# Performance work log

Measured on AMD Instinct MI355X. Metric: run time of the kernel, lower is better.

The kernel has to match this reference:

```python
import jax, jax.numpy as jnp
import numpy as np

H = 2048          # hidden_size
HEAD = 64         # head_size
NH = H // HEAD    # n_heads = 32
B, T = 4, 4096
LORA_MIX = 32     # per-branch rank of time_maa low-rank mixer (5 branches)
LORA_DECAY = 64   # rank of decay low-rank mixer


def setup_inputs() -> dict:
    key = jax.random.key(0)
    ks = jax.random.split(key, 24)
    s = 0.02  # small init scale keeps tanh/silu in sane range
    inp = {
        "hidden": jax.random.normal(ks[0], (B, T, H), jnp.float32),
        "attn_x": jax.random.normal(ks[1], (B, H), jnp.float32),
        "attn_kv": jax.random.normal(ks[2], (B, NH, HEAD, HEAD), jnp.float32),
        "ffn_x": jax.random.normal(ks[3], (B, H), jnp.float32),
        "time_maa_x": jax.random.normal(ks[4], (1, 1, H), jnp.float32) * s,
        "time_maa_w": jax.random.normal(ks[5], (1, 1, H), jnp.float32) * s,
        "time_maa_k": jax.random.normal(ks[6], (1, 1, H), jnp.float32) * s,
        "time_maa_v": jax.random.normal(ks[7], (1, 1, H), jnp.float32) * s,
        "time_maa_r": jax.random.normal(ks[8], (1, 1, H), jnp.float32) * s,
        "time_maa_g": jax.random.normal(ks[9], (1, 1, H), jnp.float32) * s,
        "time_maa_w1": jax.random.normal(ks[10], (H, LORA_MIX * 5), jnp.float32) * s,
        "time_maa_w2": jax.random.normal(ks[11], (5, LORA_MIX, H), jnp.float32) * s,
        "time_decay": jax.random.normal(ks[12], (1, 1, H), jnp.float32) * s,
        "time_decay_w1": jax.random.normal(ks[13], (H, LORA_DECAY), jnp.float32) * s,
        "time_decay_w2": jax.random.normal(ks[14], (LORA_DECAY, H), jnp.float32) * s,
        "time_faaaa": jax.random.normal(ks[15], (NH, HEAD), jnp.float32) * s,
        "receptance_w": jax.random.normal(ks[16], (H, H), jnp.float32) * s,
        "key_w": jax.random.normal(ks[17], (H, H), jnp.float32) * s,
        "value_w": jax.random.normal(ks[18], (H, H), jnp.float32) * s,
        "gate_w": jax.random.normal(ks[19], (H, H), jnp.float32) * s,
        "output_w": jax.random.normal(ks[20], (H, H), jnp.float32) * s,
    }
    return inp


def reference(hidden, attn_x, attn_kv, ffn_x,
              time_maa_x, time_maa_w, time_maa_k, time_maa_v, time_maa_r, time_maa_g,
              time_maa_w1, time_maa_w2,
              time_decay, time_decay_w1, time_decay_w2, time_faaaa,
              receptance_w, key_w, value_w, gate_w, output_w):
    b, t, h = hidden.shape
    # token shift: prepend previous chunk's last token state
    shifted = jnp.concatenate([attn_x[:, None, :], hidden[:, :-1, :]], axis=1)  # [B,T,H]
    x = hidden
    xx = shifted - x
    # low-rank data-dependent mixing coefficients (5 branches)
    xxx = x + xx * time_maa_x                                        # [B,T,H]
    xxx = jnp.tanh(xxx.reshape(-1, h) @ time_maa_w1)                 # [B*T, 5*32]
    xxx = xxx.reshape(-1, 5, LORA_MIX).transpose(1, 0, 2)            # [5, B*T, 32]
    xxx = jnp.einsum('fnr,frh->fnh', xxx, time_maa_w2)               # [5, B*T, H]
    xxx = xxx.reshape(5, b, t, h)
    mw, mk, mv, mr, mg = xxx[0], xxx[1], xxx[2], xxx[3], xxx[4]
    # note: source uses additive mix (x + xx + coeff), faithful to code as written
    td_in = x + xx + (time_maa_w + mw)
    k_in = x + xx + (time_maa_k + mk)
    v_in = x + xx + (time_maa_v + mv)
    r_in = x + xx + (time_maa_r + mr)
    g_in = x + xx + (time_maa_g + mg)
    receptance = jnp.einsum('bth,hd->btd', r_in, receptance_w)
    key = jnp.einsum('bth,hd->btd', k_in, key_w)
    value = jnp.einsum('bth,hd->btd', v_in, value_w)
    gate = jax.nn.silu(jnp.einsum('bth,hd->btd', g_in, gate_w))
    td = jnp.tanh(jnp.einsum('bth,hr->btr', td_in, time_decay_w1))
    td = jnp.einsum('btr,rh->bth', td, time_decay_w2)
    td = time_decay + td                                              # [B,T,H] per-channel decay
    attn_x_new = hidden[:, -1]                                        # [B,H]
    return (receptance, key, value, gate, td, attn_x_new)
```

## Files before the change

### kernel.cpp

```cpp
#include <hip/hip_runtime.h>

#define H 2048
#define TT 4096
#define BB 4
#define NROWS (BB * TT)
#define NTH ((size_t)NROWS * H)
#define KCAT (H + 32)
#define KC8  (H + 64)
#define NTH64 ((size_t)NROWS * 64)

typedef __attribute__((ext_vector_type(8))) short bh8;
typedef __attribute__((ext_vector_type(4))) float f32x4;

__device__ inline unsigned short f2bf(float f) {
    union { float f; unsigned u; } v; v.f = f;
    unsigned r = v.u + 0x7fff + ((v.u >> 16) & 1);
    return (unsigned short)(r >> 16);
}
__device__ inline float bf2f(unsigned short u) {
    union { unsigned u; float f; } v; v.u = ((unsigned)u) << 16; return v.f;
}
__device__ inline void gload_lds16(const void* g, void* l) {
    __builtin_amdgcn_global_load_lds(
        (const __attribute__((address_space(1))) void*)g,
        (__attribute__((address_space(3))) void*)l, 16, 0, 0);
}

__global__ __launch_bounds__(256) void prep_kernel(
    const float* __restrict__ hidden, const float* __restrict__ attn_x,
    const float* __restrict__ tmx,
    unsigned short* __restrict__ shifted, unsigned short* __restrict__ xin) {
    size_t i = ((size_t)blockIdx.x * 256 + threadIdx.x) * 4;
    int n = (int)(i >> 11);
    int h = (int)(i & 2047);
    int t = n & (TT - 1);
    float4 x = *(const float4*)(hidden + i);
    float4 s;
    if (t == 0) {
        int b = n >> 12;
        s = *(const float4*)(attn_x + ((size_t)b << 11) + h);
    } else {
        s = *(const float4*)(hidden + (i - H));
    }
    float4 m = *(const float4*)(tmx + h);
    ushort4 sh, xi;
    sh.x = f2bf(s.x); sh.y = f2bf(s.y); sh.z = f2bf(s.z); sh.w = f2bf(s.w);
    xi.x = f2bf(x.x + (s.x - x.x) * m.x);
    xi.y = f2bf(x.y + (s.y - x.y) * m.y);
    xi.z = f2bf(x.z + (s.z - x.z) * m.z);
    xi.w = f2bf(x.w + (s.w - x.w) * m.w);
    *(ushort4*)(shifted + i) = sh;
    *(ushort4*)(xin + i) = xi;
}

__global__ __launch_bounds__(256) void transpose_kernel(
    const float* __restrict__ in, unsigned short* __restrict__ outp,
    int R, int C, int ldo) {
    __shared__ float tile[32][33];
    int tx = threadIdx.x & 31, ty = threadIdx.x >> 5;
    int r0 = blockIdx.y * 32, c0 = blockIdx.x * 32;
    for (int i = ty; i < 32; i += 8) {
        int r = r0 + i, c = c0 + tx;
        tile[i][tx] = (r < R && c < C) ? in[(size_t)r * C + c] : 0.f;
    }
    __syncthreads();
    for (int i = ty; i < 32; i += 8) {
        int c = c0 + i, r = r0 + tx;
        if (c < C && r < R) outp[(size_t)c * ldo + r] = f2bf(tile[tx][i]);
    }
}

__global__ __launch_bounds__(256) void transpose4_kernel(
    const float* __restrict__ w0, const float* __restrict__ w1,
    const float* __restrict__ w2, const float* __restrict__ w3,
    unsigned short* __restrict__ d0, unsigned short* __restrict__ d1,
    unsigned short* __restrict__ d2, unsigned short* __restrict__ d3) {
    __shared__ float tile[32][33];
    int bz = blockIdx.z;
    const float* in = bz == 0 ? w0 : bz == 1 ? w1 : bz == 2 ? w2 : w3;
    unsigned short* outp = bz == 0 ? d0 : bz == 1 ? d1 : bz == 2 ? d2 : d3;
    int tx = threadIdx.x & 31, ty = threadIdx.x >> 5;
    int r0 = blockIdx.y * 32, c0 = blockIdx.x * 32;
    for (int i = ty; i < 32; i += 8)
        tile[i][tx] = in[(size_t)(r0 + i) * H + c0 + tx];
    __syncthreads();
    for (int i = ty; i < 32; i += 8)
        outp[(size_t)(c0 + i) * KC8 + r0 + tx] = f2bf(tile[tx][i]);
}

__global__ __launch_bounds__(256) void w2wp_kernel(
    const float* __restrict__ W2,
    const float* __restrict__ w0, const float* __restrict__ w1,
    const float* __restrict__ w2, const float* __restrict__ w3,
    const float* __restrict__ W1d,
    float* __restrict__ part) {
    const int br = blockIdx.z, ks = blockIdx.y, dblk = blockIdx.x;
    const int tid = threadIdx.x;
    const float* W; int D;
    if (br < 4) { W = br == 0 ? w0 : br == 1 ? w1 : br == 2 ? w2 : w3; D = H; }
    else        { W = W1d; D = 64; }
    const int f = br < 4 ? ((0x4213 >> (br * 4)) & 15) : 0;
    const float* W2f = W2 + (size_t)f * 32 * H;
    __shared__ float w2s[256][32];
    const int k0 = ks * 256;
    for (int idx = tid; idx < 8192; idx += 256) {
        int r = idx & 31, kk = idx >> 5;
        w2s[kk][r] = W2f[(size_t)r * H + k0 + kk];
    }
    __syncthreads();
    int d = dblk * 256 + tid;
    if (d >= D) return;
    float a[32];
#pragma unroll
    for (int r = 0; r < 32; ++r) a[r] = 0.f;
    for (int kk = 0; kk < 256; ++kk) {
        float w = W[(size_t)(k0 + kk) * D + d];
        const float4* w4 = (const float4*)w2s[kk];
#pragma unroll
        for (int rq = 0; rq < 8; ++rq) {
            float4 v = w4[rq];
            a[rq * 4 + 0] += v.x * w;
            a[rq * 4 + 1] += v.y * w;
            a[rq * 4 + 2] += v.z * w;
            a[rq * 4 + 3] += v.w * w;
        }
    }
    float* pp = part + (((size_t)br * 8 + ks) * 32) * 2048 + d;
#pragma unroll
    for (int r = 0; r < 32; ++r) pp[(size_t)r * 2048] = a[r];
}

__global__ __launch_bounds__(256) void w2wr_kernel(
    const float* __restrict__ part,
    unsigned short* __restrict__ dR, unsigned short* __restrict__ dK,
    unsigned short* __restrict__ dV, unsigned short* __restrict__ dG,
    unsigned short* __restrict__ d1) {
    int gid = blockIdx.x * 256 + threadIdx.x;
    if (gid < 262144) {
        int br = gid >> 16, rem = gid & 65535;
        int r = rem >> 11, d = rem & 2047;
        float s = 0.f;
#pragma unroll
        for (int ks = 0; ks < 8; ++ks)
            s += part[(((size_t)br * 8 + ks) * 32 + r) * 2048 + d];
        unsigned short* dst = br == 0 ? dR : br == 1 ? dK : br == 2 ? dV : dG;
        dst[(size_t)d * KC8 + H + r] = f2bf(s);
        dst[(size_t)d * KC8 + H + 32 + r] = 0;
    } else {
        int q = gid - 262144;
        int r = q >> 6, d = q & 63;
        float s = 0.f;
#pragma unroll
        for (int ks = 0; ks < 8; ++ks)
            s += part[(((size_t)4 * 8 + ks) * 32 + r) * 2048 + d];
        d1[(size_t)d * KCAT + H + r] = f2bf(s);
    }
}

__global__ __launch_bounds__(256) void bias_all_kernel(
    const unsigned short* __restrict__ bR, const unsigned short* __restrict__ bK,
    const unsigned short* __restrict__ bV, const unsigned short* __restrict__ bG,
    const unsigned short* __restrict__ b1,
    const float* __restrict__ mR, const float* __restrict__ mK,
    const float* __restrict__ mV, const float* __restrict__ mG,
    const float* __restrict__ mW,
    float* __restrict__ bias4, float* __restrict__ bias0) {
    int wave = threadIdx.x >> 6, lane = threadIdx.x & 63;
    int p = blockIdx.x * 4 + wave;
    const unsigned short* src; const float* maa; float* dst;
    if (p < 8192) {
        int br = p >> 11, row = p & 2047;
        src = (br == 0 ? bR : br == 1 ? bK : br == 2 ? bV : bG) + (size_t)row * KC8;
        maa = (br == 0 ? mR : br == 1 ? mK : br == 2 ? mV : mG);
        dst = bias4 + br * H + row;
    } else {
        int q = p - 8192;
        if (q >= 64) return;
        src = b1 + (size_t)q * KCAT; maa = mW; dst = bias0 + q;
    }
    float a = 0.f;
#pragma unroll 4
    for (int i = 0; i < 32; ++i) { int h = i * 64 + lane; a += bf2f(src[h]) * maa[h]; }
    for (int s = 32; s; s >>= 1) a += __shfl_xor(a, s);
    if (lane == 0) *dst = a;
}

template <int WM, int WN, int FM, int FN, int HAS_BIAS, int ACT, int OF32, int ZPAD>
__global__ __launch_bounds__(256) void gemm_kernel(
    const unsigned short* __restrict__ A, int lda,
    const unsigned short* __restrict__ A2, int lda2, int KS,
    const unsigned short* __restrict__ Bt, int ldb, int K,
    void* __restrict__ outp, int ldo, int NT,
    const float* __restrict__ bias) {
    static_assert(WM * WN == 4, "4 waves");
    constexpr int BM = WM * FM * 16;
    constexpr int BN = WN * FN * 16;
    __shared__ unsigned short As[BM * 32];
    __shared__ unsigned short Bs[BN * 32];

    const int nb = gridDim.x;
    const int bid = blockIdx.x;
    const int swz = (bid & 7) * (nb >> 3) + (bid >> 3);
    const int mt = swz / NT, nt = swz % NT;
    const int m0 = mt * BM, n0 = nt * BN;

    const int tid = threadIdx.x;
    const int wave = tid >> 6, lane = tid & 63;
    const int l16 = lane & 15, kh = lane >> 4;
    const int wr = wave / WN, wc = wave % WN;

    f32x4 acc[FM][FN] = {};

    constexpr int ACH = BM * 4;
    constexpr int BCH = BN * 4;

    for (int k0 = 0; k0 < K; k0 += 32) {
#pragma unroll
        for (int i = 0; i < (ACH + 255) / 256; ++i) {
            int c = i * 256 + tid;
            if (ACH % 256 == 0 || c < ACH) {
                int row = c >> 2, ck = c & 3;
                int kk = k0 + ck * 8;
                const unsigned short* gp = (kk < KS)
                    ? A  + (size_t)(m0 + row) * lda  + kk
                    : A2 + (size_t)(m0 + row) * lda2 + (kk - KS);
                gload_lds16(gp, As + (size_t)(i * 256 + wave * 64) * 8);
            }
        }
#pragma unroll
        for (int i = 0; i < (BCH + 255) / 256; ++i) {
            int c = i * 256 + tid;
            if (BCH % 256 == 0 || c < BCH) {
                int row = c >> 2, ck = c & 3;
                gload_lds16(Bt + (size_t)(n0 + row) * ldb + k0 + ck * 8,
                            Bs + (size_t)(i * 256 + wave * 64) * 8);
            }
        }
        __syncthreads();
        bh8 av[FM], bv[FN];
#pragma unroll
        for (int mi = 0; mi < FM; ++mi)
            av[mi] = *(const bh8*)((const char*)As + (((wr * FM + mi) * 16 + l16) * 64 + kh * 16));
#pragma unroll
        for (int ni = 0; ni < FN; ++ni)
            bv[ni] = *(const bh8*)((const char*)Bs + (((wc * FN + ni) * 16 + l16) * 64 + kh * 16));
#pragma unroll
        for (int mi = 0; mi < FM; ++mi)
#pragma unroll
            for (int ni = 0; ni < FN; ++ni)
                acc[mi][ni] = __builtin_amdgcn_mfma_f32_16x16x32_bf16(
                    av[mi], bv[ni], acc[mi][ni], 0, 0, 0);
        __syncthreads();
    }

#pragma unroll
    for (int mi = 0; mi < FM; ++mi) {
#pragma unroll
        for (int ni = 0; ni < FN; ++ni) {
            int col = n0 + (wc * FN + ni) * 16 + l16;
            float bcol = HAS_BIAS ? bias[col] : 0.f;
#pragma unroll
            for (int j = 0; j < 4; ++j) {
                int row = m0 + (wr * FM + mi) * 16 + kh * 4 + j;
                float v = acc[mi][ni][j] + bcol;
                if (ACT == 1) v = v * (1.f / (1.f + __expf(-v)));
                else if (ACT == 2) v = tanhf(v);
                if (ZPAD) {
                    int br = col >> 5, cc = col & 31;
                    unsigned short* zp = (unsigned short*)outp
                        + (size_t)br * NTH64 + (size_t)row * 64 + cc;
                    zp[0] = f2bf(v);
                    zp[32] = 0;
                } else if (OF32) {
                    ((float*)outp)[(size_t)row * ldo + col] = v;
                } else {
                    ((unsigned short*)outp)[(size_t)row * ldo + col] = f2bf(v);
                }
            }
        }
    }
}

__global__ __launch_bounds__(512, 2) void bigproj8_kernel(
    const unsigned short* __restrict__ A,
    const unsigned short* __restrict__ zpad,
    const unsigned short* __restrict__ bt0, const unsigned short* __restrict__ bt1,
    const unsigned short* __restrict__ bt2, const unsigned short* __restrict__ bt3,
    const float* __restrict__ bias4, float* __restrict__ out) {
    constexpr int BUFB = 65536;
    constexpr int NTK = KC8 / 64;
    __shared__ alignas(16) char lds[2 * BUFB];

    const int bid = blockIdx.x;
    const int swz = (bid & 7) * 256 + (bid >> 3);
    const int branch = swz >> 9;
    const int tile = swz & 511;
    const int m0 = (tile >> 3) * 256, n0 = (tile & 7) * 256;

    const unsigned short* Bt = branch == 0 ? bt0 : branch == 1 ? bt1
                             : branch == 2 ? bt2 : bt3;
    const int f = (0x4213 >> (branch * 4)) & 15;
    const unsigned short* Az = zpad + (size_t)f * NTH64;

    const int tid = threadIdx.x;
    const int wave = tid >> 6, lane = tid & 63;
    const int l16 = lane & 15, kh = lane >> 4;
    const int wm = wave >> 2, wn = wave & 3;
    const int kh16 = kh * 16;
    const int swr = (l16 & 8) << 2;

    const int rS = tid >> 2;
    const int kbx = ((tid & 3) * 16) ^ ((rS & 8) << 2);
    const char* bA0 = (const char*)A  + (size_t)(m0 + rS) * 4096 + kbx;
    const char* bA1 = bA0 + (size_t)128 * 4096;
    const char* bz0 = (const char*)Az + (size_t)(m0 + rS) * 128 + kbx;
    const char* bz1 = bz0 + (size_t)128 * 128;
    const char* bB0 = (const char*)Bt + (size_t)(n0 + rS) * (KC8 * 2) + kbx;
    const char* bB1 = bB0 + (size_t)128 * (KC8 * 2);
    const int dA0 = wave * 1024, dA1 = 8192 + wave * 1024;

    auto stageA = [&](int kt, char* nb) {
        const char *p0, *p1;
        if (kt < 32) { size_t o = (size_t)kt * 128; p0 = bA0 + o; p1 = bA1 + o; }
        else         { p0 = bz0; p1 = bz1; }
#pragma unroll
        for (int s = 0; s < 2; ++s) {
            gload_lds16(p0 + s * 64, nb + s * 16384 + dA0);
            gload_lds16(p1 + s * 64, nb + s * 16384 + dA1);
        }
    };
    auto stageB = [&](int kt, char* nb) {
        size_t o = (size_t)kt * 128;
#pragma unroll
        for (int s = 0; s < 2; ++s) {
            gload_lds16(bB0 + o + s * 64, nb + 32768 + s * 16384 + dA0);
            gload_lds16(bB1 + o + s * 64, nb + 32768 + s * 16384 + dA1);
        }
    };
    auto rdA = [&](const char* bb, int s, int g) {
        return *(const bh8*)(bb + s * 16384 + g * 1024 + l16 * 64 + (kh16 ^ swr));
    };
    auto rdB = [&](const char* bb, int s, int g) {
        return *(const bh8*)(bb + 32768 + s * 16384 + g * 1024 + l16 * 64 + (kh16 ^ swr));
    };

    f32x4 acc[8][4] = {};
    bh8 avX[4], avY[4], bv0[4], bv1[4];

    stageA(0, lds);        stageB(0, lds);
    stageA(1, lds + BUFB); stageB(1, lds + BUFB);
    asm volatile("s_waitcnt vmcnt(8)" ::: "memory");
    __builtin_amdgcn_s_barrier();
    __builtin_amdgcn_sched_barrier(0);
#pragma unroll
    for (int i = 0; i < 4; ++i) {
        avX[i] = rdA(lds, 0, wm * 8 + i);
        bv0[i] = rdB(lds, 0, wn * 4 + i);
    }

    for (int t = 0; t < NTK; ++t) {
        const char* cb = lds + (t & 1) * BUFB;
        char* sb = lds + (t & 1) * BUFB;
        const char* nxb = lds + ((t + 1) & 1) * BUFB;
        const bool hasNext = (t + 1) < NTK;
        const bool doSt = (t + 2) < NTK;

#pragma unroll
        for (int i = 0; i < 4; ++i) avY[i] = rdA(cb, 0, wm * 8 + 4 + i);
        __builtin_amdgcn_s_setprio(1);
#pragma unroll
        for (int mi = 0; mi < 4; ++mi)
#pragma unroll
            for (int ni = 0; ni < 4; ++ni)
                acc[mi][ni] = __builtin_amdgcn_mfma_f32_16x16x32_bf16(
                    avX[mi], bv0[ni], acc[mi][ni], 0, 0, 0);
        __builtin_amdgcn_s_setprio(0);

#pragma unroll
        for (int i = 0; i < 4; ++i) {
            avX[i] = rdA(cb, 1, wm * 8 + i);
            bv1[i] = rdB(cb, 1, wn * 4 + i);
        }
        __builtin_amdgcn_s_setprio(1);
#pragma unroll
        for (int mi = 0; mi < 4; ++mi)
#pragma unroll
            for (int ni = 0; ni < 4; ++ni)
                acc[4 + mi][ni] = __builtin_amdgcn_mfma_f32_16x16x32_bf16(
                    avY[mi], bv0[ni], acc[4 + mi][ni], 0, 0, 0);
        __builtin_amdgcn_s_setprio(0);

#pragma unroll
        for (int i = 0; i < 4; ++i) avY[i] = rdA(cb, 1, wm * 8 + 4 + i);
        __builtin_amdgcn_s_setprio(1);
#pragma unroll
        for (int mi = 0; mi < 4; ++mi)
#pragma unroll
            for (int ni = 0; ni < 4; ++ni)
                acc[mi][ni] = __builtin_amdgcn_mfma_f32_16x16x32_bf16(
                    avX[mi], bv1[ni], acc[mi][ni], 0, 0, 0);
        __builtin_amdgcn_s_setprio(0);

        if (hasNext) {
            asm volatile("s_waitcnt vmcnt(0) lgkmcnt(0)" ::: "memory");
            __builtin_amdgcn_s_barrier();
            __builtin_amdgcn_sched_barrier(0);
            if (doSt) { stageA(t + 2, sb); stageB(t + 2, sb); }
#pragma unroll
            for (int i = 0; i < 4; ++i) {
                avX[i] = rdA(nxb, 0, wm * 8 + i);
                bv0[i] = rdB(nxb, 0, wn * 4 + i);
            }
        }
        __builtin_amdgcn_s_setprio(1);
#pragma unroll
        for (int mi = 0; mi < 4; ++mi)
#pragma unroll
            for (int ni = 0; ni < 4; ++ni)
                acc[4 + mi][ni] = __builtin_amdgcn_mfma_f32_16x16x32_bf16(
                    avY[mi], bv1[ni], acc[4 + mi][ni], 0, 0, 0);
        __builtin_amdgcn_s_setprio(0);
    }

    float* outp = out + (size_t)branch * NTH;
    const float* bias = bias4 + branch * H;
#pragma unroll
    for (int a = 0; a < 8; ++a) {
#pragma unroll
        for (int b = 0; b < 4; ++b) {
            int col = n0 + wn * 64 + b * 16 + l16;
            float bc = bias[col];
#pragma unroll
            for (int j = 0; j < 4; ++j) {
                int row = m0 + wm * 128 + a * 16 + kh * 4 + j;
                float v = acc[a][b][j] + bc;
                if (branch == 3) v = v * (1.f / (1.f + __expf(-v)));
                outp[(size_t)row * H + col] = v;
            }
        }
    }
}

__global__ __launch_bounds__(256) void td2_kernel(
    const float* __restrict__ tdmid, const float* __restrict__ W2d,
    const float* __restrict__ tdecay, float* __restrict__ outp) {
    int col = blockIdx.x * 256 + threadIdx.x;
    int row0 = blockIdx.y * 8;
    float a[8] = {0, 0, 0, 0, 0, 0, 0, 0};
    for (int r = 0; r < 64; ++r) {
        float w = W2d[(size_t)r * H + col];
#pragma unroll
        for (int j = 0; j < 8; ++j)
            a[j] += tdmid[(size_t)(row0 + j) * 64 + r] * w;
    }
    float b = tdecay[col];
#pragma unroll
    for (int j = 0; j < 8; ++j)
        outp[(size_t)(row0 + j) * H + col] = a[j] + b;
}

__global__ __launch_bounds__(256) void axnew_kernel(
    const float* __restrict__ hidden, float* __restrict__ outp) {
    int i = blockIdx.x * 256 + threadIdx.x;
    int b = i >> 11, h = i & 2047;
    outp[i] = hidden[((size_t)(b * TT + (TT - 1)) << 11) + h];
}

extern "C" void kernel_launch(void* const* d_in, const int* in_sizes, int n_in,
                              void* d_out, int out_size, void* d_ws, size_t ws_size,
                              hipStream_t stream) {
    const float* hidden = (const float*)d_in[0];
    const float* attn_x = (const float*)d_in[1];
    const float* tmx    = (const float*)d_in[4];
    const float* tmaa_w = (const float*)d_in[5];
    const float* tmaa_k = (const float*)d_in[6];
    const float* tmaa_v = (const float*)d_in[7];
    const float* tmaa_r = (const float*)d_in[8];
    const float* tmaa_g = (const float*)d_in[9];
    const float* W1     = (const float*)d_in[10];
    const float* W2     = (const float*)d_in[11];
    const float* tdecay = (const float*)d_in[12];
    const float* W1d    = (const float*)d_in[13];
    const float* W2d    = (const float*)d_in[14];
    const float* Wr     = (const float*)d_in[16];
    const float* Wk     = (const float*)d_in[17];
    const float* Wv     = (const float*)d_in[18];
    const float* Wg     = (const float*)d_in[19];

    float* out = (float*)d_out;

    char* ws = (char*)d_ws;
    size_t off = 0;
    auto alloc = [&](size_t bytes) {
        char* p = ws + off;
        off = (off + bytes + 255) & ~(size_t)255;
        return p;
    };
    unsigned short* shifted = (unsigned short*)alloc(NTH * 2);
    unsigned short* xin     = (unsigned short*)alloc(NTH * 2);
    unsigned short* zpad    = (unsigned short*)alloc(5 * NTH64 * 2);
    unsigned short* W1t     = (unsigned short*)alloc((size_t)160 * H * 2);
    unsigned short* BcatR   = (unsigned short*)alloc((size_t)H * KC8 * 2);
    unsigned short* BcatK   = (unsigned short*)alloc((size_t)H * KC8 * 2);
    unsigned short* BcatV   = (unsigned short*)alloc((size_t)H * KC8 * 2);
    unsigned short* BcatG   = (unsigned short*)alloc((size_t)H * KC8 * 2);
    unsigned short* Bcat1   = (unsigned short*)alloc((size_t)64 * KCAT * 2);
    float* tdmid            = (float*)alloc((size_t)NROWS * 64 * 4);
    float* part             = (float*)alloc((size_t)5 * 8 * 32 * 2048 * 4);
    float* bias4            = (float*)alloc(4 * H * 4);
    float* bias0            = (float*)alloc(64 * 4);

    prep_kernel<<<(unsigned)(NTH / (4 * 256)), 256, 0, stream>>>(hidden, attn_x, tmx, shifted, xin);

    transpose4_kernel<<<dim3(64, 64, 4), 256, 0, stream>>>(
        Wr, Wk, Wv, Wg, BcatR, BcatK, BcatV, BcatG);
    transpose_kernel<<<dim3(5, 64), 256, 0, stream>>>(W1, W1t, H, 160, H);
    transpose_kernel<<<dim3(2, 64), 256, 0, stream>>>(W1d, Bcat1, H, 64, KCAT);
    w2wp_kernel<<<dim3(8, 8, 5), 256, 0, stream>>>(
        W2, Wr, Wk, Wv, Wg, W1d, part);
    w2wr_kernel<<<1032, 256, 0, stream>>>(
        part, BcatR, BcatK, BcatV, BcatG, Bcat1);
    bias_all_kernel<<<2064, 256, 0, stream>>>(
        BcatR, BcatK, BcatV, BcatG, Bcat1,
        tmaa_r, tmaa_k, tmaa_v, tmaa_g, tmaa_w, bias4, bias0);

    gemm_kernel<4, 1, 1, 10, 0, 2, 0, 1><<<256, 256, 0, stream>>>(
        xin, H, xin, H, H, W1t, H, H, zpad, 0, 1, nullptr);

    bigproj8_kernel<<<2048, 512, 0, stream>>>(
        shifted, zpad, BcatR, BcatK, BcatV, BcatG, bias4, out);

    gemm_kernel<4, 1, 1, 4, 1, 2, 1, 0><<<256, 256, 0, stream>>>(
        shifted, H, zpad, 64, H, Bcat1, KCAT, KCAT,
        tdmid, 64, 1, bias0);
    td2_kernel<<<dim3(8, NROWS / 8), 256, 0, stream>>>(
        tdmid, W2d, tdecay, out + 4 * NTH);

    axnew_kernel<<<32, 256, 0, stream>>>(hidden, out + 5 * NTH);
}
```

Baseline: 905.7 us.

## Load B operand directly from global into registers, shrink LDS to 4-stage A ring

The big projection GEMM stops staging the weight (B) tile through LDS. Each wave now reads its B fragments straight from global memory into registers, double-buffered across K steps. Only A is staged, in a 4-deep ring of 16KB buffers with a K-step of 32 instead of 64, which cuts LDS use and allows one barrier per step with partial vmcnt waits. The trade-off is redundant global/L2 traffic for B across the wm wave rows, twice as many loop iterations and barriers, and uncoalesced row-strided B loads.

```diff
diff --git a/kernel.cpp b/kernel.cpp
--- a/kernel.cpp
+++ b/kernel.cpp
@@ -287,9 +287,9 @@
     const unsigned short* __restrict__ bt0, const unsigned short* __restrict__ bt1,
     const unsigned short* __restrict__ bt2, const unsigned short* __restrict__ bt3,
     const float* __restrict__ bias4, float* __restrict__ out) {
-    constexpr int BUFB = 65536;
-    constexpr int NTK = KC8 / 64;
-    __shared__ alignas(16) char lds[2 * BUFB];
+    constexpr int BUFB = 16384;
+    constexpr int NTK = KC8 / 32;
+    __shared__ alignas(16) char lds[4 * BUFB];
 
     const int bid = blockIdx.x;
     const int swz = (bid & 7) * 256 + (bid >> 3);
@@ -315,111 +315,81 @@
     const char* bA1 = bA0 + (size_t)128 * 4096;
     const char* bz0 = (const char*)Az + (size_t)(m0 + rS) * 128 + kbx;
     const char* bz1 = bz0 + (size_t)128 * 128;
-    const char* bB0 = (const char*)Bt + (size_t)(n0 + rS) * (KC8 * 2) + kbx;
-    const char* bB1 = bB0 + (size_t)128 * (KC8 * 2);
     const int dA0 = wave * 1024, dA1 = 8192 + wave * 1024;
+
+    const char* bvBase = (const char*)Bt
+        + (size_t)(n0 + wn * 64 + l16) * (KC8 * 2) + kh16;
 
     auto stageA = [&](int kt, char* nb) {
         const char *p0, *p1;
-        if (kt < 32) { size_t o = (size_t)kt * 128; p0 = bA0 + o; p1 = bA1 + o; }
-        else         { p0 = bz0; p1 = bz1; }
-#pragma unroll
-        for (int s = 0; s < 2; ++s) {
-            gload_lds16(p0 + s * 64, nb + s * 16384 + dA0);
-            gload_lds16(p1 + s * 64, nb + s * 16384 + dA1);
+        if (kt < 64) { size_t o = (size_t)kt * 64;        p0 = bA0 + o; p1 = bA1 + o; }
+        else         { size_t o = (size_t)(kt - 64) * 64; p0 = bz0 + o; p1 = bz1 + o; }
+        gload_lds16(p0, nb + dA0);
+        gload_lds16(p1, nb + dA1);
+    };
+    auto rdA = [&](const char* bb, int g) {
+        return *(const bh8*)(bb + g * 1024 + l16 * 64 + (kh16 ^ swr));
+    };
+    auto loadBv = [&](int kt, bh8 (&bv)[4]) {
+#pragma unroll
+        for (int i = 0; i < 4; ++i)
+            bv[i] = *(const bh8*)(bvBase + (size_t)i * (16 * KC8 * 2) + (size_t)kt * 64);
+    };
+
+    f32x4 acc[8][4] = {};
+    bh8 avX[4], avY[4], bvA[4], bvB[4];
+
+    stageA(0, lds);
+    loadBv(0, bvA);
+    __builtin_amdgcn_sched_barrier(0);
+    stageA(1, lds + BUFB);
+    asm volatile("s_waitcnt vmcnt(2)" ::: "memory");
+    __builtin_amdgcn_s_barrier();
+    __builtin_amdgcn_sched_barrier(0);
+#pragma unroll
+    for (int i = 0; i < 4; ++i) avX[i] = rdA(lds, wm * 8 + i);
+
+    auto tile_step = [&](int t, bh8 (&bvC)[4], bh8 (&bvN)[4]) {
+        const char* cb = lds + (t & 3) * BUFB;
+        const bool hasNext = (t + 1) < NTK;
+        const bool doSt = (t + 2) < NTK;
+
+#pragma unroll
+        for (int i = 0; i < 4; ++i) avY[i] = rdA(cb, wm * 8 + 4 + i);
+        if (hasNext) loadBv(t + 1, bvN);
+        __builtin_amdgcn_sched_barrier(0);
+        if (doSt) stageA(t + 2, lds + ((t + 2) & 3) * BUFB);
+        __builtin_amdgcn_s_setprio(1);
+#pragma unroll
+        for (int mi = 0; mi < 4; ++mi)
+#pragma unroll
+            for (int ni = 0; ni < 4; ++ni)
+                acc[mi][ni] = __builtin_amdgcn_mfma_f32_16x16x32_bf16(
+                    avX[mi], bvC[ni], acc[mi][ni], 0, 0, 0);
+        __builtin_amdgcn_s_setprio(0);
+
+        __builtin_amdgcn_s_setprio(1);
+#pragma unroll
+        for (int mi = 0; mi < 4; ++mi)
+#pragma unroll
+            for (int ni = 0; ni < 4; ++ni)
+                acc[4 + mi][ni] = __builtin_amdgcn_mfma_f32_16x16x32_bf16(
+                    avY[mi], bvC[ni], acc[4 + mi][ni], 0, 0, 0);
+        __builtin_amdgcn_s_setprio(0);
+        if (hasNext) {
+            if (doSt) asm volatile("s_waitcnt vmcnt(2)" ::: "memory");
+            else      asm volatile("s_waitcnt vmcnt(0)" ::: "memory");
+            __builtin_amdgcn_s_barrier();
+            __builtin_amdgcn_sched_barrier(0);
+            const char* nxb = lds + ((t + 1) & 3) * BUFB;
+#pragma unroll
+            for (int i = 0; i < 4; ++i) avX[i] = rdA(nxb, wm * 8 + i);
         }
     };
-    auto stageB = [&](int kt, char* nb) {
-        size_t o = (size_t)kt * 128;
-#pragma unroll
-        for (int s = 0; s < 2; ++s) {
-            gload_lds16(bB0 + o + s * 64, nb + 32768 + s * 16384 + dA0);
-            gload_lds16(bB1 + o + s * 64, nb + 32768 + s * 16384 + dA1);
-        }
-    };
-    auto rdA = [&](const char* bb, int s, int g) {
-        return *(const bh8*)(bb + s * 16384 + g * 1024 + l16 * 64 + (kh16 ^ swr));
-    };
-    auto rdB = [&](const char* bb, int s, int g) {
-        return *(const bh8*)(bb + 32768 + s * 16384 + g * 1024 + l16 * 64 + (kh16 ^ swr));
-    };
-
-    f32x4 acc[8][4] = {};
-    bh8 avX[4], avY[4], bv0[4], bv1[4];
-
-    stageA(0, lds);        stageB(0, lds);
-    stageA(1, lds + BUFB); stageB(1, lds + BUFB);
-    asm volatile("s_waitcnt vmcnt(8)" ::: "memory");
-    __builtin_amdgcn_s_barrier();
-    __builtin_amdgcn_sched_barrier(0);
-#pragma unroll
-    for (int i = 0; i < 4; ++i) {
-        avX[i] = rdA(lds, 0, wm * 8 + i);
-        bv0[i] = rdB(lds, 0, wn * 4 + i);
-    }
-
-    for (int t = 0; t < NTK; ++t) {
-        const char* cb = lds + (t & 1) * BUFB;
-        char* sb = lds + (t & 1) * BUFB;
-        const char* nxb = lds + ((t + 1) & 1) * BUFB;
-        const bool hasNext = (t + 1) < NTK;
-        const bool doSt = (t + 2) < NTK;
-
-#pragma unroll
-        for (int i = 0; i < 4; ++i) avY[i] = rdA(cb, 0, wm * 8 + 4 + i);
-        __builtin_amdgcn_s_setprio(1);
-#pragma unroll
-        for (int mi = 0; mi < 4; ++mi)
-#pragma unroll
-            for (int ni = 0; ni < 4; ++ni)
-                acc[mi][ni] = __builtin_amdgcn_mfma_f32_16x16x32_bf16(
-                    avX[mi], bv0[ni], acc[mi][ni], 0, 0, 0);
-        __builtin_amdgcn_s_setprio(0);
-
-#pragma unroll
-        for (int i = 0; i < 4; ++i) {
-            avX[i] = rdA(cb, 1, wm * 8 + i);
-            bv1[i] = rdB(cb, 1, wn * 4 + i);
-        }
-        __builtin_amdgcn_s_setprio(1);
-#pragma unroll
-        for (int mi = 0; mi < 4; ++mi)
-#pragma unroll
-            for (int ni = 0; ni < 4; ++ni)
-                acc[4 + mi][ni] = __builtin_amdgcn_mfma_f32_16x16x32_bf16(
-                    avY[mi], bv0[ni], acc[4 + mi][ni], 0, 0, 0);
-        __builtin_amdgcn_s_setprio(0);
-
-#pragma unroll
-        for (int i = 0; i < 4; ++i) avY[i] = rdA(cb, 1, wm * 8 + 4 + i);
-        __builtin_amdgcn_s_setprio(1);
-#pragma unroll
-        for (int mi = 0; mi < 4; ++mi)
-#pragma unroll
-            for (int ni = 0; ni < 4; ++ni)
-                acc[mi][ni] = __builtin_amdgcn_mfma_f32_16x16x32_bf16(
-                    avX[mi], bv1[ni], acc[mi][ni], 0, 0, 0);
-        __builtin_amdgcn_s_setprio(0);
-
-        if (hasNext) {
-            asm volatile("s_waitcnt vmcnt(0) lgkmcnt(0)" ::: "memory");
-            __builtin_amdgcn_s_barrier();
-            __builtin_amdgcn_sched_barrier(0);
-            if (doSt) { stageA(t + 2, sb); stageB(t + 2, sb); }
-#pragma unroll
-            for (int i = 0; i < 4; ++i) {
-                avX[i] = rdA(nxb, 0, wm * 8 + i);
-                bv0[i] = rdB(nxb, 0, wn * 4 + i);
-            }
-        }
-        __builtin_amdgcn_s_setprio(1);
-#pragma unroll
-        for (int mi = 0; mi < 4; ++mi)
-#pragma unroll
-            for (int ni = 0; ni < 4; ++ni)
-                acc[4 + mi][ni] = __builtin_amdgcn_mfma_f32_16x16x32_bf16(
-                    avY[mi], bv1[ni], acc[4 + mi][ni], 0, 0, 0);
-        __builtin_amdgcn_s_setprio(0);
+
+    for (int t = 0; t < NTK; t += 2) {
+        tile_step(t,     bvA, bvB);
+        tile_step(t + 1, bvB, bvA);
     }
 
     float* outp = out + (size_t)branch * NTH;
```

New measurement: 1.334 ms. 47.3% more time.
